# Optimization experiments

Measured on AMD Instinct MI355X. Metric: run time of the kernel, lower is better.

## Reference

```python
import jax, jax.numpy as jnp
import numpy as np

DIM = 256
NUM_ITERS = 5
NUM_CLASSES = 365
TRIU_LEN = DIM * (DIM + 1) // 2  # 32896

# lower-triangular (incl. diag) flat indices in row-major order, matching
# torch.ones(d,d).triu().t().reshape(-1).nonzero()
_TRIL_IDX = np.nonzero(np.tril(np.ones((DIM, DIM), np.bool_)).reshape(-1))[0]


def setup_inputs() -> dict:
    key = jax.random.key(0)
    k1, k2 = jax.random.split(key)
    B = 64
    x = jax.random.normal(k1, (B, DIM, 14, 14), dtype=jnp.float32)
    fc_w = jax.random.normal(k2, (NUM_CLASSES, TRIU_LEN), dtype=jnp.float32) * 0.01
    fc_b = jnp.zeros((NUM_CLASSES,), dtype=jnp.float32)
    return {"x": x, "fc_w": fc_w, "fc_b": fc_b}


def _cov(x):
    # x: [B, D, H, W] -> centered second-order pooling [B, D, D]
    B, D, H, W = x.shape
    M = H * W
    xf = x.reshape(B, D, M)
    xc = xf - jnp.mean(xf, axis=2, keepdims=True)
    # x @ I_hat @ x^T == (xc @ xf^T) / M == (xc @ xc^T) / M
    y = jnp.einsum('bdm,bem->bde', xc, xc) / M
    return y + 1e-7 * jnp.eye(D, dtype=x.dtype)


def _matrix_sqrt_ns(a, num_iters):
    # Newton-Schulz iteration for matrix square root; a: [B, D, D]
    B, D, _ = a.shape
    I = jnp.eye(D, dtype=a.dtype)
    normA = jnp.trace(a, axis1=1, axis2=2)  # [B]
    Y = a / normA[:, None, None]
    Z = jnp.broadcast_to(I, (B, D, D))
    for _ in range(num_iters):
        T = 0.5 * (3.0 * I - jnp.einsum('bij,bjk->bik', Z, Y))
        Y = jnp.einsum('bij,bjk->bik', Y, T)
        Z = jnp.einsum('bij,bjk->bik', T, Z)
    return Y * jnp.sqrt(normA)[:, None, None]


def _triu(x):
    # gather lower-tri (== upper-tri of symmetric cov) entries: [B, D, D] -> [B, D(D+1)/2]
    B, D, _ = x.shape
    return x.reshape(B, D * D)[:, _TRIL_IDX]


def reference(x, fc_w, fc_b):
    y = _cov(x)
    y = _matrix_sqrt_ns(y, NUM_ITERS)
    y = _triu(y)
    return y @ fc_w.T + fc_b
```

## Files before the change

### kernel.cpp

```cpp
#include <hip/hip_runtime.h>
#include <hip/hip_bf16.h>

typedef __attribute__((ext_vector_type(8))) short bf16x8;
typedef __attribute__((ext_vector_type(4))) float f32x4;

static __device__ __forceinline__ ushort f2b(float f) {
    unsigned u = __float_as_uint(f);
    return (ushort)((u + 0x7fffu + ((u >> 16) & 1u)) >> 16);
}

static __device__ __forceinline__ void gload16(const void* g, void* lds) {
    __builtin_amdgcn_global_load_lds(
        (const __attribute__((address_space(1))) unsigned int*)g,
        (__attribute__((address_space(3))) unsigned int*)lds, 16, 0, 0);
}

__global__ __launch_bounds__(256) void prep_kernel(
    const float* __restrict__ x, ushort* __restrict__ xc, float* __restrict__ var)
{
    const int t = threadIdx.x, wv = t >> 6, l = t & 63;
    const int bid = blockIdx.x;
    const int x8 = bid & 7, rr = bid >> 3;
    const int dgrp = rr & 63, bgrp = rr >> 6;
    const int b = bgrp * 8 + x8;
    const int rowid = b * 256 + dgrp * 4 + wv;
    const float* xr = x + (size_t)rowid * 196;

    float x0 = xr[l];
    float x1 = xr[l + 64];
    float x2 = xr[l + 128];
    float x3 = (l < 4) ? xr[l + 192] : 0.0f;

    float s1 = x0 + x1 + x2 + x3;
    float s2 = x0*x0 + x1*x1 + x2*x2 + x3*x3;
    #pragma unroll
    for (int off = 32; off; off >>= 1) {
        s1 += __shfl_xor(s1, off);
        s2 += __shfl_xor(s2, off);
    }
    const float mean = s1 * (1.0f / 196.0f);
    if (l == 0) var[rowid] = s2 * (1.0f / 196.0f) - mean * mean + 1e-7f;

    ushort* xcr = xc + (size_t)rowid * 256;
    xcr[l]       = f2b(x0 - mean);
    xcr[l + 64]  = f2b(x1 - mean);
    xcr[l + 128] = f2b(x2 - mean);
    xcr[l + 192] = (l < 4) ? f2b(x3 - mean) : (ushort)0;
}

template<int H>
static __device__ __forceinline__ void stage_half(
    const ushort* Ab, const ushort* Btb, int i0, int j0,
    int wv, int lrow, int seg, ushort* As, ushort* Bs)
{
    #pragma unroll
    for (int it = 0; it < 8; ++it) {
        const int c = H * 32 + wv * 8 + it;
        const int tk = c >> 3, r16 = c & 7;
        const int row = r16 * 16 + lrow;
        gload16(Ab + (size_t)(i0 + row) * 256 + tk * 32 + seg,
                (char*)As + tk * 8192 + r16 * 1024);
        gload16(Btb + (size_t)(j0 + row) * 256 + tk * 32 + seg,
                (char*)Bs + tk * 8192 + r16 * 1024);
    }
}

template<int MODE>
__global__ __launch_bounds__(256) void gemm_ns(
    const ushort* __restrict__ A, const ushort* __restrict__ A2,
    const ushort* __restrict__ Bt,
    ushort* __restrict__ C, ushort* __restrict__ C2,
    const float* __restrict__ var)
{
    __shared__ ushort As[8][128][32];
    __shared__ ushort Bs[8][128][32];
    __shared__ float tr_s[4];

    const int bid = blockIdx.x, x8 = bid & 7;
    int b, i0, j0;
    bool useA2 = false;
    if (MODE == 2) {
        const int tt = (bid >> 3) & 3;
        useA2 = ((bid >> 5) & 1) != 0;
        b = (bid >> 6) * 8 + x8;
        i0 = (tt >> 1) * 128; j0 = (tt & 1) * 128;
    } else if (MODE == 3) {
        const int rr = bid >> 3, t3 = rr % 3;
        b = (rr / 3) * 8 + x8;
        i0 = (t3 == 0) ? 0 : 128;
        j0 = (t3 == 2) ? 128 : 0;
    } else {
        const int tt = (bid >> 3) & 3;
        b = (bid >> 5) * 8 + x8;
        i0 = (tt >> 1) * 128; j0 = (tt & 1) * 128;
    }
    const ushort* Ab  = (useA2 ? A2 : A) + (size_t)b * 65536;
    const ushort* Btb = Bt + (size_t)b * 65536;

    const int t = threadIdx.x, wv = t >> 6, l = t & 63;
    const int li = l & 15, hi = l >> 4;
    const int wr = wv >> 1, wc = wv & 1;
    const int lrow = l >> 2;
    const int seg = (l & 3) * 8;

    stage_half<0>(Ab, Btb, i0, j0, wv, lrow, seg, &As[0][0][0], &Bs[0][0][0]);

    if (MODE == 0 || MODE == 3) {
        float v = var[b * 256 + t];
        #pragma unroll
        for (int off = 32; off; off >>= 1) v += __shfl_xor(v, off);
        if (l == 0) tr_s[wv] = v;
    }
    __syncthreads();
    float trace = 0.f;
    if (MODE == 0 || MODE == 3) trace = tr_s[0] + tr_s[1] + tr_s[2] + tr_s[3];

    f32x4 acc[4][4];
    #pragma unroll
    for (int m = 0; m < 4; ++m)
        #pragma unroll
        for (int n = 0; n < 4; ++n) acc[m][n] = (f32x4){0.f, 0.f, 0.f, 0.f};

    stage_half<1>(Ab, Btb, i0, j0, wv, lrow, seg, &As[0][0][0], &Bs[0][0][0]);

    #pragma unroll
    for (int tk = 0; tk < 4; ++tk) {
        bf16x8 af[4], bfr[4];
        #pragma unroll
        for (int m = 0; m < 4; ++m)
            af[m] = *(const bf16x8*)&As[tk][wr * 64 + m * 16 + li][hi * 8];
        #pragma unroll
        for (int n = 0; n < 4; ++n)
            bfr[n] = *(const bf16x8*)&Bs[tk][wc * 64 + n * 16 + li][hi * 8];
        #pragma unroll
        for (int m = 0; m < 4; ++m)
            #pragma unroll
            for (int n = 0; n < 4; ++n)
                acc[m][n] = __builtin_amdgcn_mfma_f32_16x16x32_bf16(
                    af[m], bfr[n], acc[m][n], 0, 0, 0);
    }
    __syncthreads();
    #pragma unroll
    for (int tk = 4; tk < 8; ++tk) {
        bf16x8 af[4], bfr[4];
        #pragma unroll
        for (int m = 0; m < 4; ++m)
            af[m] = *(const bf16x8*)&As[tk][wr * 64 + m * 16 + li][hi * 8];
        #pragma unroll
        for (int n = 0; n < 4; ++n)
            bfr[n] = *(const bf16x8*)&Bs[tk][wc * 64 + n * 16 + li][hi * 8];
        #pragma unroll
        for (int m = 0; m < 4; ++m)
            #pragma unroll
            for (int n = 0; n < 4; ++n)
                acc[m][n] = __builtin_amdgcn_mfma_f32_16x16x32_bf16(
                    af[m], bfr[n], acc[m][n], 0, 0, 0);
    }

    if (MODE == 3) {
        const float sc = sqrtf(trace);
        ushort* trib = C + (size_t)b * 32896;
        #pragma unroll
        for (int m = 0; m < 4; ++m)
            #pragma unroll
            for (int n = 0; n < 4; ++n)
                #pragma unroll
                for (int r = 0; r < 4; ++r) {
                    const int gi = i0 + wr * 64 + m * 16 + hi * 4 + r;
                    const int gj = j0 + wc * 64 + n * 16 + li;
                    if (gj <= gi)
                        trib[(gi * (gi + 1)) / 2 + gj] = f2b(acc[m][n][r] * sc);
                }
    } else {
        const float invtr = (MODE == 0) ? (1.0f / trace) : 0.0f;
        ushort* Cb  = ((MODE == 2 && useA2) ? C2 : C) + (size_t)b * 65536;
        ushort* C2b = (MODE == 0) ? (C2 + (size_t)b * 65536) : nullptr;
        #pragma unroll
        for (int m = 0; m < 4; ++m)
            #pragma unroll
            for (int n = 0; n < 4; ++n)
                #pragma unroll
                for (int r = 0; r < 4; ++r) {
                    const int gi = i0 + wr * 64 + m * 16 + hi * 4 + r;
                    const int gj = j0 + wc * 64 + n * 16 + li;
                    const float v = acc[m][n][r];
                    const size_t idx = (size_t)gi * 256 + gj;
                    if (MODE == 0) {
                        float y0 = (v * (1.0f / 196.0f) + ((gi == gj) ? 1e-7f : 0.0f)) * invtr;
                        Cb[idx]  = f2b(y0);
                        C2b[idx] = f2b(((gi == gj) ? 1.5f : 0.0f) - 0.5f * y0);
                    } else if (MODE == 1) {
                        Cb[idx] = f2b(((gi == gj) ? 1.5f : 0.0f) - 0.5f * v);
                    } else {
                        Cb[idx] = f2b(v);
                    }
                }
    }
}

__global__ __launch_bounds__(256) void fc_gemm(
    const ushort* __restrict__ tri, const float* __restrict__ W,
    float* __restrict__ partial)
{
    __shared__ ushort As[64][40];
    __shared__ ushort Bs[64][40];

    const int ntile = blockIdx.x;
    const int split = blockIdx.y;
    const int steps = 16 + (split < 4 ? 1 : 0);
    const int step0 = split * 16 + (split < 4 ? split : 4);

    const int t   = threadIdx.x;
    const int row = t >> 2, seg = t & 3;
    const int wv  = t >> 6, l = t & 63;
    const int li  = l & 15, hi = l >> 4;
    const int n   = ntile * 64 + row;

    f32x4 acc[4];
    #pragma unroll
    for (int c = 0; c < 4; ++c) acc[c] = (f32x4){0.f, 0.f, 0.f, 0.f};

    for (int s = 0; s < steps; ++s) {
        const int kk = (step0 + s) * 32;
        *(bf16x8*)&As[row][seg * 8] =
            *(const bf16x8*)(tri + (size_t)row * 32896 + kk + seg * 8);
        bf16x8 pk;
        if (n < 365) {
            const float* wp = W + (size_t)n * 32896 + kk + seg * 8;
            float4 f0 = *(const float4*)wp;
            float4 f1 = *(const float4*)(wp + 4);
            pk[0] = (short)f2b(f0.x); pk[1] = (short)f2b(f0.y);
            pk[2] = (short)f2b(f0.z); pk[3] = (short)f2b(f0.w);
            pk[4] = (short)f2b(f1.x); pk[5] = (short)f2b(f1.y);
            pk[6] = (short)f2b(f1.z); pk[7] = (short)f2b(f1.w);
        } else {
            pk = (bf16x8){0,0,0,0,0,0,0,0};
        }
        *(bf16x8*)&Bs[row][seg * 8] = pk;
        __syncthreads();
        bf16x8 a = *(const bf16x8*)&As[wv * 16 + li][hi * 8];
        #pragma unroll
        for (int c = 0; c < 4; ++c) {
            bf16x8 bb = *(const bf16x8*)&Bs[c * 16 + li][hi * 8];
            acc[c] = __builtin_amdgcn_mfma_f32_16x16x32_bf16(a, bb, acc[c], 0, 0, 0);
        }
        __syncthreads();
    }

    #pragma unroll
    for (int c = 0; c < 4; ++c) {
        #pragma unroll
        for (int r = 0; r < 4; ++r) {
            const int i = wv * 16 + hi * 4 + r;
            const int j = ntile * 64 + c * 16 + li;
            partial[((size_t)split * 64 + i) * 384 + j] = acc[c][r];
        }
    }
}

__global__ void fc_reduce(const float* __restrict__ partial,
                          const float* __restrict__ bias, float* __restrict__ out)
{
    const int idx = blockIdx.x * 256 + threadIdx.x;
    if (idx >= 64 * 365) return;
    const int b = idx / 365, n = idx % 365;
    float s = bias[n];
    #pragma unroll 4
    for (int sp = 0; sp < 64; ++sp)
        s += partial[((size_t)sp * 64 + b) * 384 + n];
    out[idx] = s;
}

extern "C" void kernel_launch(void* const* d_in, const int* in_sizes, int n_in,
                              void* d_out, int out_size, void* d_ws, size_t ws_size,
                              hipStream_t stream)
{
    const float* x   = (const float*)d_in[0];
    const float* fcw = (const float*)d_in[1];
    const float* fcb = (const float*)d_in[2];
    float* out = (float*)d_out;
    char* ws = (char*)d_ws;

    const size_t MS = (size_t)64 * 256 * 256 * 2;
    ushort* w0 = (ushort*)(ws + 0 * MS);
    ushort* w1 = (ushort*)(ws + 1 * MS);
    ushort* w2 = (ushort*)(ws + 2 * MS);
    ushort* w3 = (ushort*)(ws + 3 * MS);
    ushort* w4 = (ushort*)(ws + 4 * MS);
    ushort* xc = (ushort*)(ws + 5 * MS);
    float*  var    = (float*)(ws + 6 * MS);
    ushort* tri    = (ushort*)(ws + 6 * MS + 131072);
    float*  partial= (float*)(ws + 6 * MS + 131072 + 4210688);

    prep_kernel<<<4096, 256, 0, stream>>>(x, xc, var);

    gemm_ns<0><<<256, 256, 0, stream>>>(xc, nullptr, xc, w0, w1, var);
    gemm_ns<4><<<256, 256, 0, stream>>>(w0, nullptr, w1, w2, nullptr, nullptr);
    gemm_ns<1><<<256, 256, 0, stream>>>(w1, nullptr, w2, w0, nullptr, nullptr);
    gemm_ns<2><<<512, 256, 0, stream>>>(w2, w1, w0, w3, w4, nullptr);
    gemm_ns<1><<<256, 256, 0, stream>>>(w4, nullptr, w3, w0, nullptr, nullptr);
    gemm_ns<2><<<512, 256, 0, stream>>>(w3, w4, w0, w1, w2, nullptr);
    gemm_ns<1><<<256, 256, 0, stream>>>(w2, nullptr, w1, w0, nullptr, nullptr);
    gemm_ns<2><<<512, 256, 0, stream>>>(w1, w2, w0, w3, w4, nullptr);
    gemm_ns<1><<<256, 256, 0, stream>>>(w4, nullptr, w3, w0, nullptr, nullptr);
    gemm_ns<3><<<192, 256, 0, stream>>>(w3, nullptr, w0, tri, nullptr, var);

    fc_gemm<<<dim3(6, 64), 256, 0, stream>>>(tri, fcw, partial);
    fc_reduce<<<(64 * 365 + 255) / 256, 256, 0, stream>>>(partial, fcb, out);
}
```

Baseline: 124.3 us.

## Fuse prep and Newton-Schulz chain into one persistent kernel with per-batch spin barriers

Replaces the prep kernel and ten separate GEMM launches with a single persistent kernel. The four tile blocks of each batch coordinate through atomic counters and spin-waits instead of kernel boundaries. Each block reuses an already staged LDS panel, computing Z·T as (T^T-like) swapped operands, to avoid reloads. The FC split-K is also doubled to 128 splits. This removes launch gaps and tail effects, at the cost of relying on all 256 blocks being co-resident for the spin barriers, which adds deadlock risk.

```diff
diff --git a/kernel.cpp b/kernel.cpp
--- a/kernel.cpp
+++ b/kernel.cpp
@@ -15,186 +15,248 @@
         (__attribute__((address_space(3))) unsigned int*)lds, 16, 0, 0);
 }
 
-__global__ __launch_bounds__(256) void prep_kernel(
-    const float* __restrict__ x, ushort* __restrict__ xc, float* __restrict__ var)
-{
-    const int t = threadIdx.x, wv = t >> 6, l = t & 63;
-    const int bid = blockIdx.x;
-    const int x8 = bid & 7, rr = bid >> 3;
-    const int dgrp = rr & 63, bgrp = rr >> 6;
-    const int b = bgrp * 8 + x8;
-    const int rowid = b * 256 + dgrp * 4 + wv;
-    const float* xr = x + (size_t)rowid * 196;
-
-    float x0 = xr[l];
-    float x1 = xr[l + 64];
-    float x2 = xr[l + 128];
-    float x3 = (l < 4) ? xr[l + 192] : 0.0f;
-
-    float s1 = x0 + x1 + x2 + x3;
-    float s2 = x0*x0 + x1*x1 + x2*x2 + x3*x3;
+#define MS ((size_t)8 << 20)
+#define TRI_OFF ((size_t)14 * MS)
+#define VAR_OFF ((size_t)122 << 20)
+#define CNT_OFF (VAR_OFF + 65536)
+#define PART_OFF ((size_t)123 << 20)
+
+static __device__ __forceinline__ void sig_add(int* cb) {
+    __hip_atomic_fetch_add(cb, 1, __ATOMIC_RELEASE, __HIP_MEMORY_SCOPE_AGENT);
+}
+static __device__ __forceinline__ void spin_until(int* cb, int tgt) {
+    while (__hip_atomic_load(cb, __ATOMIC_RELAXED, __HIP_MEMORY_SCOPE_AGENT) < tgt)
+        __builtin_amdgcn_s_sleep(1);
+    (void)__hip_atomic_load(cb, __ATOMIC_ACQUIRE, __HIP_MEMORY_SCOPE_AGENT);
+}
+
+static __device__ __forceinline__ void stage_panel(
+    const ushort* __restrict__ rows, void* panel, int wv, int l)
+{
+    const int lrow = l >> 2;
+    const int seg = (l & 3) * 8;
     #pragma unroll
-    for (int off = 32; off; off >>= 1) {
-        s1 += __shfl_xor(s1, off);
-        s2 += __shfl_xor(s2, off);
-    }
-    const float mean = s1 * (1.0f / 196.0f);
-    if (l == 0) var[rowid] = s2 * (1.0f / 196.0f) - mean * mean + 1e-7f;
-
-    ushort* xcr = xc + (size_t)rowid * 256;
-    xcr[l]       = f2b(x0 - mean);
-    xcr[l + 64]  = f2b(x1 - mean);
-    xcr[l + 128] = f2b(x2 - mean);
-    xcr[l + 192] = (l < 4) ? f2b(x3 - mean) : (ushort)0;
-}
-
-template<int H>
-static __device__ __forceinline__ void stage_half(
-    const ushort* Ab, const ushort* Btb, int i0, int j0,
-    int wv, int lrow, int seg, ushort* As, ushort* Bs)
-{
-    #pragma unroll
-    for (int it = 0; it < 8; ++it) {
-        const int c = H * 32 + wv * 8 + it;
+    for (int it = 0; it < 16; ++it) {
+        const int c = wv * 16 + it;
         const int tk = c >> 3, r16 = c & 7;
         const int row = r16 * 16 + lrow;
-        gload16(Ab + (size_t)(i0 + row) * 256 + tk * 32 + seg,
-                (char*)As + tk * 8192 + r16 * 1024);
-        gload16(Btb + (size_t)(j0 + row) * 256 + tk * 32 + seg,
-                (char*)Bs + tk * 8192 + r16 * 1024);
-    }
-}
-
-template<int MODE>
-__global__ __launch_bounds__(256) void gemm_ns(
-    const ushort* __restrict__ A, const ushort* __restrict__ A2,
-    const ushort* __restrict__ Bt,
-    ushort* __restrict__ C, ushort* __restrict__ C2,
-    const float* __restrict__ var)
+        gload16(rows + (size_t)row * 256 + tk * 32 + seg,
+                (char*)panel + tk * 8192 + r16 * 1024);
+    }
+}
+
+static __device__ __forceinline__ void compute_tile(
+    const ushort (&Ap)[8][128][32], const ushort (&Bp)[8][128][32],
+    f32x4 (&acc)[4][4], int wr, int wc, int li, int hi)
+{
+    #pragma unroll
+    for (int tk = 0; tk < 8; ++tk) {
+        bf16x8 af[4], bfr[4];
+        #pragma unroll
+        for (int m = 0; m < 4; ++m)
+            af[m] = *(const bf16x8*)&Ap[tk][wr * 64 + m * 16 + li][hi * 8];
+        #pragma unroll
+        for (int n = 0; n < 4; ++n)
+            bfr[n] = *(const bf16x8*)&Bp[tk][wc * 64 + n * 16 + li][hi * 8];
+        #pragma unroll
+        for (int m = 0; m < 4; ++m)
+            #pragma unroll
+            for (int n = 0; n < 4; ++n)
+                acc[m][n] = __builtin_amdgcn_mfma_f32_16x16x32_bf16(
+                    af[m], bfr[n], acc[m][n], 0, 0, 0);
+    }
+}
+
+#define ZERO_ACC do { _Pragma("unroll") for (int m = 0; m < 4; ++m) \
+    _Pragma("unroll") for (int n = 0; n < 4; ++n) acc[m][n] = (f32x4){0.f,0.f,0.f,0.f}; } while (0)
+
+__global__ __launch_bounds__(256) void ns_chain(
+    const float* __restrict__ x, char* __restrict__ ws)
 {
     __shared__ ushort As[8][128][32];
     __shared__ ushort Bs[8][128][32];
     __shared__ float tr_s[4];
 
-    const int bid = blockIdx.x, x8 = bid & 7;
-    int b, i0, j0;
-    bool useA2 = false;
-    if (MODE == 2) {
-        const int tt = (bid >> 3) & 3;
-        useA2 = ((bid >> 5) & 1) != 0;
-        b = (bid >> 6) * 8 + x8;
-        i0 = (tt >> 1) * 128; j0 = (tt & 1) * 128;
-    } else if (MODE == 3) {
-        const int rr = bid >> 3, t3 = rr % 3;
-        b = (rr / 3) * 8 + x8;
-        i0 = (t3 == 0) ? 0 : 128;
-        j0 = (t3 == 2) ? 128 : 0;
-    } else {
-        const int tt = (bid >> 3) & 3;
-        b = (bid >> 5) * 8 + x8;
-        i0 = (tt >> 1) * 128; j0 = (tt & 1) * 128;
-    }
-    const ushort* Ab  = (useA2 ? A2 : A) + (size_t)b * 65536;
-    const ushort* Btb = Bt + (size_t)b * 65536;
-
-    const int t = threadIdx.x, wv = t >> 6, l = t & 63;
-    const int li = l & 15, hi = l >> 4;
-    const int wr = wv >> 1, wc = wv & 1;
-    const int lrow = l >> 2;
-    const int seg = (l & 3) * 8;
-
-    stage_half<0>(Ab, Btb, i0, j0, wv, lrow, seg, &As[0][0][0], &Bs[0][0][0]);
-
-    if (MODE == 0 || MODE == 3) {
-        float v = var[b * 256 + t];
-        #pragma unroll
-        for (int off = 32; off; off >>= 1) v += __shfl_xor(v, off);
-        if (l == 0) tr_s[wv] = v;
-    }
-    __syncthreads();
-    float trace = 0.f;
-    if (MODE == 0 || MODE == 3) trace = tr_s[0] + tr_s[1] + tr_s[2] + tr_s[3];
+    const int blk = blockIdx.x;
+    const int x8 = blk & 7, t = (blk >> 3) & 3, bhi = blk >> 5;
+    const int b = bhi * 8 + x8;
+    const int i0 = (t >> 1) * 128, j0 = (t & 1) * 128;
+    const int tid = threadIdx.x, wv = tid >> 6, l = tid & 63;
+    const int li = l & 15, hi = l >> 4, wr = wv >> 1, wc = wv & 1;
+    const size_t bo = (size_t)b * 65536;
+
+    ushort* xc = (ushort*)ws;
+    float* var = (float*)(ws + VAR_OFF);
+    int* cb = (int*)(ws + CNT_OFF) + b;
+    ushort* tri = (ushort*)(ws + TRI_OFF);
+
+    #pragma unroll 2
+    for (int rr = 0; rr < 16; ++rr) {
+        const int row = t * 64 + rr * 4 + wv;
+        const float* xr = x + ((size_t)b * 256 + row) * 196;
+        float x0 = xr[l], x1 = xr[l + 64], x2 = xr[l + 128];
+        float x3 = (l < 4) ? xr[l + 192] : 0.0f;
+        float s1 = x0 + x1 + x2 + x3;
+        float s2 = x0 * x0 + x1 * x1 + x2 * x2 + x3 * x3;
+        #pragma unroll
+        for (int off = 32; off; off >>= 1) {
+            s1 += __shfl_xor(s1, off);
+            s2 += __shfl_xor(s2, off);
+        }
+        const float mean = s1 * (1.0f / 196.0f);
+        if (l == 0) var[b * 256 + row] = s2 * (1.0f / 196.0f) - mean * mean + 1e-7f;
+        ushort* xcr = xc + bo + (size_t)row * 256;
+        xcr[l]       = f2b(x0 - mean);
+        xcr[l + 64]  = f2b(x1 - mean);
+        xcr[l + 128] = f2b(x2 - mean);
+        xcr[l + 192] = (l < 4) ? f2b(x3 - mean) : (ushort)0;
+    }
+    __syncthreads();
+    if (tid == 0) { sig_add(cb); spin_until(cb, 4); }
+    __syncthreads();
+
+    stage_panel(xc + bo + (size_t)i0 * 256, As, wv, l);
+    stage_panel(xc + bo + (size_t)j0 * 256, Bs, wv, l);
+    {
+        float v0 = var[b * 256 + tid];
+        #pragma unroll
+        for (int off = 32; off; off >>= 1) v0 += __shfl_xor(v0, off);
+        if (l == 0) tr_s[wv] = v0;
+    }
+    __syncthreads();
+    const float trace = tr_s[0] + tr_s[1] + tr_s[2] + tr_s[3];
+    const float invtr = 1.0f / trace;
 
     f32x4 acc[4][4];
-    #pragma unroll
-    for (int m = 0; m < 4; ++m)
-        #pragma unroll
-        for (int n = 0; n < 4; ++n) acc[m][n] = (f32x4){0.f, 0.f, 0.f, 0.f};
-
-    stage_half<1>(Ab, Btb, i0, j0, wv, lrow, seg, &As[0][0][0], &Bs[0][0][0]);
-
-    #pragma unroll
-    for (int tk = 0; tk < 4; ++tk) {
-        bf16x8 af[4], bfr[4];
-        #pragma unroll
-        for (int m = 0; m < 4; ++m)
-            af[m] = *(const bf16x8*)&As[tk][wr * 64 + m * 16 + li][hi * 8];
+    ZERO_ACC;
+    compute_tile(As, Bs, acc, wr, wc, li, hi);
+    {
+        ushort* Y0b = (ushort*)(ws + 1 * MS) + bo;
+        ushort* T0b = (ushort*)(ws + 2 * MS) + bo;
+        #pragma unroll
+        for (int m = 0; m < 4; ++m)
         #pragma unroll
         for (int n = 0; n < 4; ++n)
-            bfr[n] = *(const bf16x8*)&Bs[tk][wc * 64 + n * 16 + li][hi * 8];
-        #pragma unroll
-        for (int m = 0; m < 4; ++m)
+        #pragma unroll
+        for (int r = 0; r < 4; ++r) {
+            const int gi = i0 + wr * 64 + m * 16 + hi * 4 + r;
+            const int gj = j0 + wc * 64 + n * 16 + li;
+            const float y0 = (acc[m][n][r] * (1.0f / 196.0f)
+                              + ((gi == gj) ? 1e-7f : 0.0f)) * invtr;
+            Y0b[(size_t)gi * 256 + gj] = f2b(y0);
+            T0b[(size_t)gi * 256 + gj] = f2b(((gi == gj) ? 1.5f : 0.0f) - 0.5f * y0);
+        }
+    }
+    __syncthreads();
+    if (tid == 0) { sig_add(cb); spin_until(cb, 8); }
+    __syncthreads();
+
+    stage_panel((ushort*)(ws + 1 * MS) + bo + (size_t)i0 * 256, As, wv, l);
+    stage_panel((ushort*)(ws + 2 * MS) + bo + (size_t)j0 * 256, Bs, wv, l);
+    __syncthreads();
+    ZERO_ACC;
+    compute_tile(As, Bs, acc, wr, wc, li, hi);
+    {
+        ushort* Y1b = (ushort*)(ws + 3 * MS) + bo;
+        #pragma unroll
+        for (int m = 0; m < 4; ++m)
+        #pragma unroll
+        for (int n = 0; n < 4; ++n)
+        #pragma unroll
+        for (int r = 0; r < 4; ++r) {
+            const int gi = i0 + wr * 64 + m * 16 + hi * 4 + r;
+            const int gj = j0 + wc * 64 + n * 16 + li;
+            Y1b[(size_t)gi * 256 + gj] = f2b(acc[m][n][r]);
+        }
+    }
+    __syncthreads();
+    if (tid == 0) sig_add(cb);
+    stage_panel((ushort*)(ws + 2 * MS) + bo + (size_t)i0 * 256, As, wv, l);
+    if (tid == 0) spin_until(cb, 12);
+    __syncthreads();
+
+    int tgt = 12;
+    #pragma unroll 1
+    for (int it = 0; it < 4; ++it) {
+        const ushort* Zb = (const ushort*)(ws + (size_t)(it ? 3 * it + 3 : 2) * MS) + bo;
+        const ushort* Yb = (const ushort*)(ws + (size_t)(it ? 3 * it + 2 : 3) * MS) + bo;
+        ushort* Tb = (ushort*)(ws + (size_t)(3 * it + 4) * MS) + bo;
+
+        if (it > 0) stage_panel(Zb + (size_t)i0 * 256, As, wv, l);
+        stage_panel(Yb + (size_t)j0 * 256, Bs, wv, l);
+        __syncthreads();
+        ZERO_ACC;
+        compute_tile(As, Bs, acc, wr, wc, li, hi);
+        #pragma unroll
+        for (int m = 0; m < 4; ++m)
+        #pragma unroll
+        for (int n = 0; n < 4; ++n)
+        #pragma unroll
+        for (int r = 0; r < 4; ++r) {
+            const int gi = i0 + wr * 64 + m * 16 + hi * 4 + r;
+            const int gj = j0 + wc * 64 + n * 16 + li;
+            Tb[(size_t)gi * 256 + gj] =
+                f2b(((gi == gj) ? 1.5f : 0.0f) - 0.5f * acc[m][n][r]);
+        }
+        __syncthreads();
+        if (tid == 0) sig_add(cb);
+        stage_panel(Yb + (size_t)i0 * 256, As, wv, l);
+        tgt += 4;
+        if (tid == 0) spin_until(cb, tgt);
+        __syncthreads();
+
+        stage_panel(Tb + (size_t)j0 * 256, Bs, wv, l);
+        __syncthreads();
+        ZERO_ACC;
+        compute_tile(As, Bs, acc, wr, wc, li, hi);
+        if (it < 3) {
+            ushort* Yob = (ushort*)(ws + (size_t)(3 * it + 5) * MS) + bo;
+            #pragma unroll
+            for (int m = 0; m < 4; ++m)
             #pragma unroll
             for (int n = 0; n < 4; ++n)
-                acc[m][n] = __builtin_amdgcn_mfma_f32_16x16x32_bf16(
-                    af[m], bfr[n], acc[m][n], 0, 0, 0);
-    }
-    __syncthreads();
-    #pragma unroll
-    for (int tk = 4; tk < 8; ++tk) {
-        bf16x8 af[4], bfr[4];
-        #pragma unroll
-        for (int m = 0; m < 4; ++m)
-            af[m] = *(const bf16x8*)&As[tk][wr * 64 + m * 16 + li][hi * 8];
-        #pragma unroll
-        for (int n = 0; n < 4; ++n)
-            bfr[n] = *(const bf16x8*)&Bs[tk][wc * 64 + n * 16 + li][hi * 8];
-        #pragma unroll
-        for (int m = 0; m < 4; ++m)
+            #pragma unroll
+            for (int r = 0; r < 4; ++r) {
+                const int gi = i0 + wr * 64 + m * 16 + hi * 4 + r;
+                const int gj = j0 + wc * 64 + n * 16 + li;
+                Yob[(size_t)gi * 256 + gj] = f2b(acc[m][n][r]);
+            }
+            __syncthreads();
+            stage_panel(Zb + (size_t)i0 * 256, As, wv, l);
+            __syncthreads();
+            ZERO_ACC;
+            compute_tile(Bs, As, acc, wr, wc, li, hi);
+            ushort* Zob = (ushort*)(ws + (size_t)(3 * it + 6) * MS) + bo;
+            #pragma unroll
+            for (int m = 0; m < 4; ++m)
             #pragma unroll
             for (int n = 0; n < 4; ++n)
-                acc[m][n] = __builtin_amdgcn_mfma_f32_16x16x32_bf16(
-                    af[m], bfr[n], acc[m][n], 0, 0, 0);
-    }
-
-    if (MODE == 3) {
-        const float sc = sqrtf(trace);
-        ushort* trib = C + (size_t)b * 32896;
-        #pragma unroll
-        for (int m = 0; m < 4; ++m)
+            #pragma unroll
+            for (int r = 0; r < 4; ++r) {
+                const int gi = j0 + wr * 64 + m * 16 + hi * 4 + r;
+                const int gj = i0 + wc * 64 + n * 16 + li;
+                Zob[(size_t)gi * 256 + gj] = f2b(acc[m][n][r]);
+            }
+            __syncthreads();
+            if (tid == 0) sig_add(cb);
+            tgt += 4;
+            if (tid == 0) spin_until(cb, tgt);
+            __syncthreads();
+        } else if (t != 1) {
+            const float sc = sqrtf(trace);
+            ushort* trib = tri + (size_t)b * 32896;
+            #pragma unroll
+            for (int m = 0; m < 4; ++m)
             #pragma unroll
             for (int n = 0; n < 4; ++n)
-                #pragma unroll
-                for (int r = 0; r < 4; ++r) {
-                    const int gi = i0 + wr * 64 + m * 16 + hi * 4 + r;
-                    const int gj = j0 + wc * 64 + n * 16 + li;
-                    if (gj <= gi)
-                        trib[(gi * (gi + 1)) / 2 + gj] = f2b(acc[m][n][r] * sc);
-                }
-    } else {
-        const float invtr = (MODE == 0) ? (1.0f / trace) : 0.0f;
-        ushort* Cb  = ((MODE == 2 && useA2) ? C2 : C) + (size_t)b * 65536;
-        ushort* C2b = (MODE == 0) ? (C2 + (size_t)b * 65536) : nullptr;
-        #pragma unroll
-        for (int m = 0; m < 4; ++m)
-            #pragma unroll
-            for (int n = 0; n < 4; ++n)
-                #pragma unroll
-                for (int r = 0; r < 4; ++r) {
-                    const int gi = i0 + wr * 64 + m * 16 + hi * 4 + r;
-                    const int gj = j0 + wc * 64 + n * 16 + li;
-                    const float v = acc[m][n][r];
-                    const size_t idx = (size_t)gi * 256 + gj;
-                    if (MODE == 0) {
-                        float y0 = (v * (1.0f / 196.0f) + ((gi == gj) ? 1e-7f : 0.0f)) * invtr;
-                        Cb[idx]  = f2b(y0);
-                        C2b[idx] = f2b(((gi == gj) ? 1.5f : 0.0f) - 0.5f * y0);
-                    } else if (MODE == 1) {
-                        Cb[idx] = f2b(((gi == gj) ? 1.5f : 0.0f) - 0.5f * v);
-                    } else {
-                        Cb[idx] = f2b(v);
-                    }
-                }
+            #pragma unroll
+            for (int r = 0; r < 4; ++r) {
+                const int gi = i0 + wr * 64 + m * 16 + hi * 4 + r;
+                const int gj = j0 + wc * 64 + n * 16 + li;
+                if (gj <= gi)
+                    trib[(gi * (gi + 1)) / 2 + gj] = f2b(acc[m][n][r] * sc);
+            }
+        }
     }
 }
 
@@ -207,8 +269,8 @@
 
     const int ntile = blockIdx.x;
     const int split = blockIdx.y;
-    const int steps = 16 + (split < 4 ? 1 : 0);
-    const int step0 = split * 16 + (split < 4 ? split : 4);
+    const int steps = 8 + (split < 4 ? 1 : 0);
+    const int step0 = split * 8 + (split < 4 ? split : 4);
 
     const int t   = threadIdx.x;
     const int row = t >> 2, seg = t & 3;
@@ -266,7 +328,7 @@
     const int b = idx / 365, n = idx % 365;
     float s = bias[n];
     #pragma unroll 4
-    for (int sp = 0; sp < 64; ++sp)
+    for (int sp = 0; sp < 128; ++sp)
         s += partial[((size_t)sp * 64 + b) * 384 + n];
     out[idx] = s;
 }
@@ -275,36 +337,17 @@
                               void* d_out, int out_size, void* d_ws, size_t ws_size,
                               hipStream_t stream)
 {
+    (void)in_sizes; (void)n_in; (void)out_size; (void)ws_size;
     const float* x   = (const float*)d_in[0];
     const float* fcw = (const float*)d_in[1];
     const float* fcb = (const float*)d_in[2];
     float* out = (float*)d_out;
     char* ws = (char*)d_ws;
 
-    const size_t MS = (size_t)64 * 256 * 256 * 2;
-    ushort* w0 = (ushort*)(ws + 0 * MS);
-    ushort* w1 = (ushort*)(ws + 1 * MS);
-    ushort* w2 = (ushort*)(ws + 2 * MS);
-    ushort* w3 = (ushort*)(ws + 3 * MS);
-    ushort* w4 = (ushort*)(ws + 4 * MS);
-    ushort* xc = (ushort*)(ws + 5 * MS);
-    float*  var    = (float*)(ws + 6 * MS);
-    ushort* tri    = (ushort*)(ws + 6 * MS + 131072);
-    float*  partial= (float*)(ws + 6 * MS + 131072 + 4210688);
-
-    prep_kernel<<<4096, 256, 0, stream>>>(x, xc, var);
-
-    gemm_ns<0><<<256, 256, 0, stream>>>(xc, nullptr, xc, w0, w1, var);
-    gemm_ns<4><<<256, 256, 0, stream>>>(w0, nullptr, w1, w2, nullptr, nullptr);
-    gemm_ns<1><<<256, 256, 0, stream>>>(w1, nullptr, w2, w0, nullptr, nullptr);
-    gemm_ns<2><<<512, 256, 0, stream>>>(w2, w1, w0, w3, w4, nullptr);
-    gemm_ns<1><<<256, 256, 0, stream>>>(w4, nullptr, w3, w0, nullptr, nullptr);
-    gemm_ns<2><<<512, 256, 0, stream>>>(w3, w4, w0, w1, w2, nullptr);
-    gemm_ns<1><<<256, 256, 0, stream>>>(w2, nullptr, w1, w0, nullptr, nullptr);
-    gemm_ns<2><<<512, 256, 0, stream>>>(w1, w2, w0, w3, w4, nullptr);
-    gemm_ns<1><<<256, 256, 0, stream>>>(w4, nullptr, w3, w0, nullptr, nullptr);
-    gemm_ns<3><<<192, 256, 0, stream>>>(w3, nullptr, w0, tri, nullptr, var);
-
-    fc_gemm<<<dim3(6, 64), 256, 0, stream>>>(tri, fcw, partial);
-    fc_reduce<<<(64 * 365 + 255) / 256, 256, 0, stream>>>(partial, fcb, out);
-}
+    hipMemsetAsync(ws + CNT_OFF, 0, 512, stream);
+    ns_chain<<<256, 256, 0, stream>>>(x, ws);
+    fc_gemm<<<dim3(6, 128), 256, 0, stream>>>(
+        (const ushort*)(ws + TRI_OFF), fcw, (float*)(ws + PART_OFF));
+    fc_reduce<<<(64 * 365 + 255) / 256, 256, 0, stream>>>(
+        (const float*)(ws + PART_OFF), fcb, out);
+}
```

Result: slower. 222.4 us (+78.9%).

## Pipeline FC GEMM loads with async global-to-LDS multi-stage buffering

Applied to the files above, without the earlier changes.

Rewrites the FC GEMM inner loop to use a 4-slot LDS ring filled by asynchronous global_load_lds copies issued three steps ahead. The raw fp32 weights are kept in LDS and converted to bf16 only when fragments are read. Waves are reassigned so each wave owns one 16-column weight slice and loops over four batch row tiles. The goal is to hide global load latency, which dominates this memory-bound GEMM over a large fp32 weight matrix. The cost is more LDS use, a hand-tuned vmcnt wait, and clamped out-of-range weight rows that rely on those output columns being discarded later.

```diff
diff --git a/kernel.cpp b/kernel.cpp
--- a/kernel.cpp
+++ b/kernel.cpp
@@ -202,60 +202,75 @@
     const ushort* __restrict__ tri, const float* __restrict__ W,
     float* __restrict__ partial)
 {
-    __shared__ ushort As[64][40];
-    __shared__ ushort Bs[64][40];
+    __shared__ ushort Asl[4][64][32];
+    __shared__ float  Wsl[4][64][32];
 
     const int ntile = blockIdx.x;
     const int split = blockIdx.y;
     const int steps = 16 + (split < 4 ? 1 : 0);
     const int step0 = split * 16 + (split < 4 ? split : 4);
 
-    const int t   = threadIdx.x;
-    const int row = t >> 2, seg = t & 3;
-    const int wv  = t >> 6, l = t & 63;
-    const int li  = l & 15, hi = l >> 4;
-    const int n   = ntile * 64 + row;
+    const int tid = threadIdx.x, wv = tid >> 6, l = tid & 63;
+    const int li = l & 15, hi = l >> 4;
+
+    const int arow = tid >> 2, aseg = tid & 3;
+    const int wrow0 = tid >> 3, wseg = tid & 7;
+    const int wrow1 = 32 + (tid >> 3);
+    const int wcl0 = min(ntile * 64 + wrow0, 364);
+    const int wcl1 = min(ntile * 64 + wrow1, 364);
+
+#define FSTAGE(s) do {                                                          \
+    const int kk_ = (step0 + (s)) * 32;                                         \
+    const int r_ = (s) & 3;                                                     \
+    gload16(tri + (size_t)arow * 32896 + kk_ + aseg * 8,                        \
+            &Asl[r_][arow][aseg * 8]);                                          \
+    gload16(W + (size_t)wcl0 * 32896 + kk_ + wseg * 4,                          \
+            &Wsl[r_][wrow0][wseg * 4]);                                         \
+    gload16(W + (size_t)wcl1 * 32896 + kk_ + wseg * 4,                          \
+            &Wsl[r_][wrow1][wseg * 4]);                                         \
+} while (0)
+
+    FSTAGE(0); FSTAGE(1); FSTAGE(2);
 
     f32x4 acc[4];
     #pragma unroll
-    for (int c = 0; c < 4; ++c) acc[c] = (f32x4){0.f, 0.f, 0.f, 0.f};
+    for (int m = 0; m < 4; ++m) acc[m] = (f32x4){0.f, 0.f, 0.f, 0.f};
 
     for (int s = 0; s < steps; ++s) {
-        const int kk = (step0 + s) * 32;
-        *(bf16x8*)&As[row][seg * 8] =
-            *(const bf16x8*)(tri + (size_t)row * 32896 + kk + seg * 8);
-        bf16x8 pk;
-        if (n < 365) {
-            const float* wp = W + (size_t)n * 32896 + kk + seg * 8;
-            float4 f0 = *(const float4*)wp;
-            float4 f1 = *(const float4*)(wp + 4);
-            pk[0] = (short)f2b(f0.x); pk[1] = (short)f2b(f0.y);
-            pk[2] = (short)f2b(f0.z); pk[3] = (short)f2b(f0.w);
-            pk[4] = (short)f2b(f1.x); pk[5] = (short)f2b(f1.y);
-            pk[6] = (short)f2b(f1.z); pk[7] = (short)f2b(f1.w);
-        } else {
-            pk = (bf16x8){0,0,0,0,0,0,0,0};
+        if (s + 3 < steps) FSTAGE(s + 3);
+        asm volatile("s_waitcnt vmcnt(9)" ::: "memory");
+        __builtin_amdgcn_sched_barrier(0);
+        __builtin_amdgcn_s_barrier();
+
+        const int r = s & 3;
+        const float4 wf0 = *(const float4*)&Wsl[r][wv * 16 + li][hi * 8];
+        const float4 wf1 = *(const float4*)&Wsl[r][wv * 16 + li][hi * 8 + 4];
+        bf16x8 bfr;
+        bfr[0] = (short)f2b(wf0.x); bfr[1] = (short)f2b(wf0.y);
+        bfr[2] = (short)f2b(wf0.z); bfr[3] = (short)f2b(wf0.w);
+        bfr[4] = (short)f2b(wf1.x); bfr[5] = (short)f2b(wf1.y);
+        bfr[6] = (short)f2b(wf1.z); bfr[7] = (short)f2b(wf1.w);
+
+        bf16x8 af[4];
+        #pragma unroll
+        for (int m = 0; m < 4; ++m)
+            af[m] = *(const bf16x8*)&Asl[r][m * 16 + li][hi * 8];
+        #pragma unroll
+        for (int m = 0; m < 4; ++m)
+            acc[m] = __builtin_amdgcn_mfma_f32_16x16x32_bf16(af[m], bfr, acc[m], 0, 0, 0);
+
+        __builtin_amdgcn_s_barrier();
+    }
+#undef FSTAGE
+
+    #pragma unroll
+    for (int m = 0; m < 4; ++m)
+        #pragma unroll
+        for (int rr = 0; rr < 4; ++rr) {
+            const int i = m * 16 + hi * 4 + rr;
+            const int j = ntile * 64 + wv * 16 + li;
+            partial[((size_t)split * 64 + i) * 384 + j] = acc[m][rr];
         }
-        *(bf16x8*)&Bs[row][seg * 8] = pk;
-        __syncthreads();
-        bf16x8 a = *(const bf16x8*)&As[wv * 16 + li][hi * 8];
-        #pragma unroll
-        for (int c = 0; c < 4; ++c) {
-            bf16x8 bb = *(const bf16x8*)&Bs[c * 16 + li][hi * 8];
-            acc[c] = __builtin_amdgcn_mfma_f32_16x16x32_bf16(a, bb, acc[c], 0, 0, 0);
-        }
-        __syncthreads();
-    }
-
-    #pragma unroll
-    for (int c = 0; c < 4; ++c) {
-        #pragma unroll
-        for (int r = 0; r < 4; ++r) {
-            const int i = wv * 16 + hi * 4 + r;
-            const int j = ntile * 64 + c * 16 + li;
-            partial[((size_t)split * 64 + i) * 384 + j] = acc[c][r];
-        }
-    }
 }
 
 __global__ void fc_reduce(const float* __restrict__ partial,
@@ -275,6 +290,7 @@
                               void* d_out, int out_size, void* d_ws, size_t ws_size,
                               hipStream_t stream)
 {
+    (void)in_sizes; (void)n_in; (void)out_size; (void)ws_size;
     const float* x   = (const float*)d_in[0];
     const float* fcw = (const float*)d_in[1];
     const float* fcb = (const float*)d_in[2];
```

After: 122.8 us. Within noise of the previous version (-1.2%).
